# Performance work log

Hardware: AMD Instinct MI355X
Metric: run time of the kernel (lower is better)

The kernel has to match this reference:

```python
import jax, jax.numpy as jnp
import numpy as np

N, E, T = 4096, 49152, 262144
H, EMB, AIN, EB, TB = 256, 64, 92, 80, 40
NBLK = 12  # 4 alignn * 2 EGGC + 4 gcn


def _ln(x, s, b):
    mu = jnp.mean(x, -1, keepdims=True)
    v = jnp.mean((x - mu) ** 2, -1, keepdims=True)
    return (x - mu) * jax.lax.rsqrt(v + 1e-5) * s + b


def _mlp(x, W, b, s, bi):
    # Linear -> LayerNorm -> SiLU (MLPLayer)
    return jax.nn.silu(_ln(x @ W + b, s, bi))


def _rbf(x, vmin, vmax, bins):
    centers = jnp.linspace(vmin, vmax, bins)
    gamma = 1.0 / ((vmax - vmin) / (bins - 1))
    return jnp.exp(-gamma * (x[:, None] - centers) ** 2)


def _eggc(x, e, src, dst, W, b, ln_s, ln_b, n_nodes):
    # W: [5,H,H] = src_gate, dst_gate, edge_gate, src_update, dst_update
    m = (x @ W[0] + b[0])[src] + (x @ W[1] + b[1])[dst] + (e @ W[2] + b[2])
    sigma = jax.nn.sigmoid(m)
    sum_sh = jax.ops.segment_sum((x @ W[4] + b[4])[src] * sigma, dst, num_segments=n_nodes)
    sum_s = jax.ops.segment_sum(sigma, dst, num_segments=n_nodes)
    h = sum_sh / (sum_s + 1e-6)
    x_new = jax.nn.silu(_ln(x @ W[3] + b[3] + h, ln_s[0], ln_b[0]))
    e_new = jax.nn.silu(_ln(m, ln_s[1], ln_b[1]))
    return x + x_new, e + e_new  # residual=True


def setup_inputs() -> dict:
    key = jax.random.key(0)
    ks = jax.random.split(key, 16)
    s = 0.05
    return {
        "atom_features": jax.random.normal(ks[0], (N, AIN), jnp.float32),
        "r": jax.random.normal(ks[1], (E, 3), jnp.float32),
        "src": jax.random.randint(ks[2], (E,), 0, N),
        "dst": jax.random.randint(ks[3], (E,), 0, N),
        "lsrc": jax.random.randint(ks[4], (T,), 0, E),
        "ldst": jax.random.randint(ks[5], (T,), 0, E),
        "atom_W": s * jax.random.normal(ks[6], (AIN, H), jnp.float32),
        "atom_b": jnp.zeros((H,), jnp.float32),
        "atom_ln_s": jnp.ones((H,), jnp.float32),
        "atom_ln_b": jnp.zeros((H,), jnp.float32),
        "edge_W1": s * jax.random.normal(ks[7], (EB, EMB), jnp.float32),
        "edge_b1": jnp.zeros((EMB,), jnp.float32),
        "edge_ln1_s": jnp.ones((EMB,), jnp.float32),
        "edge_ln1_b": jnp.zeros((EMB,), jnp.float32),
        "edge_W2": s * jax.random.normal(ks[8], (EMB, H), jnp.float32),
        "edge_b2": jnp.zeros((H,), jnp.float32),
        "edge_ln2_s": jnp.ones((H,), jnp.float32),
        "edge_ln2_b": jnp.zeros((H,), jnp.float32),
        "ang_W1": s * jax.random.normal(ks[9], (TB, EMB), jnp.float32),
        "ang_b1": jnp.zeros((EMB,), jnp.float32),
        "ang_ln1_s": jnp.ones((EMB,), jnp.float32),
        "ang_ln1_b": jnp.zeros((EMB,), jnp.float32),
        "ang_W2": s * jax.random.normal(ks[10], (EMB, H), jnp.float32),
        "ang_b2": jnp.zeros((H,), jnp.float32),
        "ang_ln2_s": jnp.ones((H,), jnp.float32),
        "ang_ln2_b": jnp.zeros((H,), jnp.float32),
        "eggc_W": s * jax.random.normal(ks[11], (NBLK, 5, H, H), jnp.float32),
        "eggc_b": jnp.zeros((NBLK, 5, H), jnp.float32),
        "eggc_ln_s": jnp.ones((NBLK, 2, H), jnp.float32),
        "eggc_ln_b": jnp.zeros((NBLK, 2, H), jnp.float32),
        "fc_W": s * jax.random.normal(ks[12], (H, 1), jnp.float32),
        "fc_b": jnp.zeros((1,), jnp.float32),
    }


def reference(atom_features, r, src, dst, lsrc, ldst,
              atom_W, atom_b, atom_ln_s, atom_ln_b,
              edge_W1, edge_b1, edge_ln1_s, edge_ln1_b,
              edge_W2, edge_b2, edge_ln2_s, edge_ln2_b,
              ang_W1, ang_b1, ang_ln1_s, ang_ln1_b,
              ang_W2, ang_b2, ang_ln2_s, ang_ln2_b,
              eggc_W, eggc_b, eggc_ln_s, eggc_ln_b, fc_W, fc_b):
    # line-graph bond cosines: cos(-r_i, r_j) for each bond pair
    r1, r2 = -r[lsrc], r[ldst]
    cos = jnp.sum(r1 * r2, -1) / (jnp.linalg.norm(r1, axis=-1) * jnp.linalg.norm(r2, axis=-1))
    cos = jnp.clip(cos, -1.0, 1.0)
    z = _mlp(_mlp(_rbf(cos, -1.0, 1.0, TB), ang_W1, ang_b1, ang_ln1_s, ang_ln1_b),
             ang_W2, ang_b2, ang_ln2_s, ang_ln2_b)
    x = _mlp(atom_features, atom_W, atom_b, atom_ln_s, atom_ln_b)
    bondlength = jnp.linalg.norm(r, axis=1)
    y = _mlp(_mlp(_rbf(bondlength, 0.0, 8.0, EB), edge_W1, edge_b1, edge_ln1_s, edge_ln1_b),
             edge_W2, edge_b2, edge_ln2_s, edge_ln2_b)
    for i in range(4):  # alignn layers: crystal graph then line graph
        x, m = _eggc(x, y, src, dst, eggc_W[2 * i], eggc_b[2 * i], eggc_ln_s[2 * i], eggc_ln_b[2 * i], N)
        y, z = _eggc(m, z, lsrc, ldst, eggc_W[2 * i + 1], eggc_b[2 * i + 1], eggc_ln_s[2 * i + 1], eggc_ln_b[2 * i + 1], E)
    for i in range(4):  # gcn layers
        j = 8 + i
        x, y = _eggc(x, y, src, dst, eggc_W[j], eggc_b[j], eggc_ln_s[j], eggc_ln_b[j], N)
    atomwise_energy = x @ fc_W + fc_b  # [N,1]
    total_energy = jnp.mean(atomwise_energy)  # AvgPooling (eV/atom), single graph
    return total_energy, atomwise_energy
```

## Files before the change

kernel.cpp:

```cpp
#include <hip/hip_runtime.h>


typedef unsigned short bfu;
typedef __attribute__((ext_vector_type(8))) short short8;
typedef __attribute__((ext_vector_type(4))) float floatx4;

#define CHN 4096
#define CHCAP 24576
#define HH 65536

__device__ __forceinline__ float bf2f(bfu u) {
  union { unsigned u; float f; } x; x.u = ((unsigned)u) << 16; return x.f;
}
__device__ __forceinline__ bfu f2bf(float f) {
  union { float f; unsigned u; } x; x.f = f;
  unsigned r = x.u + 0x7FFFu + ((x.u >> 16) & 1u);
  return (bfu)(r >> 16);
}
__device__ __forceinline__ float fsig(float x) {
  return __builtin_amdgcn_rcpf(1.f + __expf(-x));
}
__device__ __forceinline__ float fsilu(float x) { return x * fsig(x); }

struct f8 { float v[8]; };
__device__ __forceinline__ f8 ld8(const bfu* p) {
  short8 u = *(const short8*)(const void*)p;
  f8 r;
#pragma unroll
  for (int i = 0; i < 8; ++i) r.v[i] = bf2f((bfu)u[i]);
  return r;
}
__device__ __forceinline__ void st8(bfu* p, f8 x) {
  short8 u;
#pragma unroll
  for (int i = 0; i < 8; ++i) u[i] = (short)f2bf(x.v[i]);
  *(short8*)(void*)p = u;
}
__device__ __forceinline__ f8 add8(f8 a, f8 b) {
  f8 r;
#pragma unroll
  for (int i = 0; i < 8; ++i) r.v[i] = a.v[i] + b.v[i];
  return r;
}
__device__ __forceinline__ f8 sig8(f8 m) {
  f8 r;
#pragma unroll
  for (int i = 0; i < 8; ++i) r.v[i] = fsig(m.v[i]);
  return r;
}
__device__ __forceinline__ void wstats32(const f8& x, float& mean, float& rstd) {
  float s = 0.f, q = 0.f;
#pragma unroll
  for (int i = 0; i < 8; ++i) { s += x.v[i]; q += x.v[i] * x.v[i]; }
#pragma unroll
  for (int m = 1; m < 32; m <<= 1) { s += __shfl_xor(s, m); q += __shfl_xor(q, m); }
  mean = s * (1.f / 256.f);
  rstd = rsqrtf(fmaxf(q * (1.f / 256.f) - mean * mean, 0.f) + 1e-5f);
}
__device__ __forceinline__ f8 lnsilu8(f8 pre, f8 sg, f8 bb) {
  float mean, rstd; wstats32(pre, mean, rstd);
  f8 r;
#pragma unroll
  for (int i = 0; i < 8; ++i)
    r.v[i] = fsilu((pre.v[i] - mean) * rstd * sg.v[i] + bb.v[i]);
  return r;
}

__device__ __forceinline__ float block_sum256(float t, float* sm) {
#pragma unroll
  for (int o = 32; o; o >>= 1) t += __shfl_down(t, o);
  if ((threadIdx.x & 63) == 0) sm[threadIdx.x >> 6] = t;
  __syncthreads();
  float r = sm[0] + sm[1] + sm[2] + sm[3];
  __syncthreads();
  return r;
}

__global__ void probe_kernel(const unsigned* __restrict__ ones_raw, int* __restrict__ mode) {
  if (threadIdx.x == 0) *mode = (ones_raw[0] == 0x3F800000u) ? 1 : 0;
}
__global__ __launch_bounds__(256) void cvt_kernel(
    const void* __restrict__ src, bfu* __restrict__ dst, int n, const int* __restrict__ mode) {
  int i = blockIdx.x * 256 + threadIdx.x;
  if (i >= n) return;
  dst[i] = (*mode) ? f2bf(((const float*)src)[i]) : ((const bfu*)src)[i];
}
__global__ __launch_bounds__(256) void cvtf_kernel(
    const void* __restrict__ src, float* __restrict__ dst, int n, const int* __restrict__ mode) {
  int i = blockIdx.x * 256 + threadIdx.x;
  if (i >= n) return;
  dst[i] = (*mode) ? ((const float*)src)[i] : bf2f(((const bfu*)src)[i]);
}
struct CvtDesc { const void* src; bfu* dst; int n; };
struct CvtPack { CvtDesc e[20]; };
__global__ __launch_bounds__(256) void cvt_batch_kernel(CvtPack p, const int* __restrict__ mode) {
  CvtDesc d = p.e[blockIdx.y];
  int i = blockIdx.x * 256 + threadIdx.x;
  if (i >= d.n) return;
  d.dst[i] = (*mode) ? f2bf(((const float*)d.src)[i]) : ((const bfu*)d.src)[i];
}

template<int BM, int BN, int WR, int WC>
__device__ __forceinline__ void gemm_body(
    const bfu* __restrict__ A, const bfu* __restrict__ Bt,
    const bfu* __restrict__ bias, bfu* __restrict__ Cout,
    int cnt, int N, int K, int base, int m0, int n0)
{
  constexpr int WM = BM / WR, WN = BN / WC;
  constexpr int TM = WM / 16, TN = WN / 16;
  constexpr int LDT = 72;
  static __shared__ bfu As[BM * LDT];
  static __shared__ bfu Bs[BN * LDT];

  const int tid = threadIdx.x, wave = tid >> 6, lane = tid & 63;
  const int wr = wave / WC, wc = wave % WC;
  const int lrow = lane & 15, kq = (lane >> 4) * 8;

  floatx4 acc[TM][TN];
#pragma unroll
  for (int i = 0; i < TM; ++i)
#pragma unroll
    for (int j = 0; j < TN; ++j) acc[i][j] = (floatx4){0.f, 0.f, 0.f, 0.f};

  constexpr int ACH = BM * 8, BCH = BN * 8;
  for (int k0 = 0; k0 < K; k0 += 64) {
#pragma unroll
    for (int idx = tid; idx < ACH; idx += 256) {
      int row = idx >> 3, kc = (idx & 7) << 3;
      int r = m0 + row;
      int ar = base + (r < cnt ? r : cnt - 1);
      *(short8*)(void*)(As + row * LDT + kc) =
          *(const short8*)(const void*)(A + (size_t)ar * K + k0 + kc);
    }
#pragma unroll
    for (int idx = tid; idx < BCH; idx += 256) {
      int row = idx >> 3, kc = (idx & 7) << 3;
      *(short8*)(void*)(Bs + row * LDT + kc) =
          *(const short8*)(const void*)(Bt + (size_t)(n0 + row) * K + k0 + kc);
    }
    __syncthreads();
#pragma unroll
    for (int s = 0; s < 2; ++s) {
      short8 Af[TM], Bf[TN];
#pragma unroll
      for (int i = 0; i < TM; ++i)
        Af[i] = *(const short8*)(const void*)(As + (wr * WM + i * 16 + lrow) * LDT + s * 32 + kq);
#pragma unroll
      for (int j = 0; j < TN; ++j)
        Bf[j] = *(const short8*)(const void*)(Bs + (wc * WN + j * 16 + lrow) * LDT + s * 32 + kq);
#pragma unroll
      for (int i = 0; i < TM; ++i)
#pragma unroll
        for (int j = 0; j < TN; ++j)
          acc[i][j] = __builtin_amdgcn_mfma_f32_16x16x32_bf16(Af[i], Bf[j], acc[i][j], 0, 0, 0);
    }
    __syncthreads();
  }

  const int rquad = lane >> 4, cin = lane & 15;
#pragma unroll
  for (int i = 0; i < TM; ++i) {
#pragma unroll
    for (int rr = 0; rr < 4; ++rr) {
      int orow = m0 + wr * WM + i * 16 + rquad * 4 + rr;
      if (orow >= cnt) continue;
#pragma unroll
      for (int j = 0; j < TN; ++j) {
        int gcol = n0 + wc * WN + j * 16 + cin;
        Cout[(size_t)orow * N + gcol] = f2bf(acc[i][j][rr] + bf2f(bias[gcol]));
      }
    }
  }
}

template<int BM, int BN, int WR, int WC>
__global__ __launch_bounds__(256) void gemm_kernel(
    const bfu* __restrict__ A, const bfu* __restrict__ Bt,
    const bfu* __restrict__ bias, bfu* __restrict__ Cout, int M, int N, int K)
{
  gemm_body<BM, BN, WR, WC>(A, Bt, bias, Cout, M, N, K, 0,
                            blockIdx.x * BM, blockIdx.y * BN);
}

__global__ __launch_bounds__(256) void line_gemm_kernel(
    const bfu* __restrict__ z, const bfu* __restrict__ yb,
    const bfu* __restrict__ W, const bfu* __restrict__ bb,
    bfu* __restrict__ mchunk, bfu* __restrict__ u3c,
    const int* __restrict__ loff, int n0, int n1)
{
  if (blockIdx.y < 2) {
    int base = loff[n0], cnt = loff[n1] - base;
    int m0 = blockIdx.x * 128;
    if (m0 >= cnt) return;
    gemm_body<128, 128, 2, 2>(z, W + 4 * HH, bb + 4 * 256, mchunk,
                              cnt, 256, 256, base, m0, blockIdx.y * 128);
  } else {
    if (blockIdx.x >= 64) return;
    gemm_body<128, 128, 2, 2>(yb + (size_t)n0 * 256, W + 3 * HH, bb + 3 * 256, u3c,
                              CHN, 256, 256, 0, (blockIdx.x & 31) * 128, (blockIdx.x >> 5) * 128);
  }
}

__global__ __launch_bounds__(256) void atom_gemm_kernel(
    const bfu* __restrict__ x, const bfu* __restrict__ y,
    const bfu* __restrict__ W, const bfu* __restrict__ bb,
    bfu* __restrict__ afused, bfu* __restrict__ mbufa)
{
  if (blockIdx.x < 384) {
    gemm_body<128, 128, 2, 2>(y, W + 4 * HH, bb + 4 * 256, mbufa,
                              49152, 256, 256, 0, blockIdx.x * 128, blockIdx.y * 128);
  } else {
    int lid = (blockIdx.x - 384) * 2 + blockIdx.y;
    gemm_body<128, 128, 2, 2>(x, W, bb, afused,
                              4096, 1024, 256, 0, (lid >> 3) * 128, (lid & 7) * 128);
  }
}

__global__ __launch_bounds__(256) void line_gates_kernel(
    const bfu* __restrict__ y, const bfu* __restrict__ z,
    const bfu* __restrict__ W, const bfu* __restrict__ bb,
    bfu* __restrict__ lfused, bfu* __restrict__ mchunk, bfu* __restrict__ u3c,
    const int* __restrict__ loff)
{
  if (blockIdx.y < 6) {
    gemm_body<128, 128, 2, 2>(y, W, bb, lfused,
                              49152, 768, 256, 0, blockIdx.x * 128, blockIdx.y * 128);
  } else if (blockIdx.y < 8) {
    int cnt = loff[CHN];
    int m0 = blockIdx.x * 128;
    if (blockIdx.x >= CHCAP / 128 || m0 >= cnt) return;
    gemm_body<128, 128, 2, 2>(z, W + 4 * HH, bb + 4 * 256, mchunk,
                              cnt, 256, 256, 0, m0, (blockIdx.y - 6) * 128);
  } else {
    if (blockIdx.x >= 64) return;
    gemm_body<128, 128, 2, 2>(y, W + 3 * HH, bb + 3 * 256, u3c,
                              CHN, 256, 256, 0, (blockIdx.x & 31) * 128, (blockIdx.x >> 5) * 128);
  }
}

__global__ __launch_bounds__(256) void cosbl_kernel(
    const float* __restrict__ r, const int* __restrict__ lsrc_p,
    const int* __restrict__ ldst_p, float* __restrict__ cosv,
    float* __restrict__ bl, int T, int E)
{
  int idx = blockIdx.x * 256 + threadIdx.x;
  if (idx < T) {
    int e1 = lsrc_p[idx], e2 = ldst_p[idx];
    float ax = -r[e1 * 3 + 0], ay = -r[e1 * 3 + 1], az = -r[e1 * 3 + 2];
    float bx =  r[e2 * 3 + 0], by =  r[e2 * 3 + 1], bz =  r[e2 * 3 + 2];
    float dot = ax * bx + ay * by + az * bz;
    float na = sqrtf(ax * ax + ay * ay + az * az);
    float nb = sqrtf(bx * bx + by * by + bz * bz);
    float c = dot / (na * nb);
    cosv[idx] = fminf(1.f, fmaxf(-1.f, c));
  } else if (idx < T + E) {
    int e = idx - T;
    float x = r[e * 3 + 0], yv = r[e * 3 + 1], zv = r[e * 3 + 2];
    bl[e] = sqrtf(x * x + yv * yv + zv * zv);
  }
}

template<int KP, int BINS, int IS_ANG>
__global__ __launch_bounds__(256) void mlp1_ln_kernel(
    const float* __restrict__ v, const bfu* __restrict__ Bt,
    const bfu* __restrict__ bias, const bfu* __restrict__ lns,
    const bfu* __restrict__ lnb, bfu* __restrict__ outp, int M)
{
  constexpr int LDT = KP + 8;
  __shared__ bfu As[128 * LDT];
  const int tid = threadIdx.x, wave = tid >> 6, lane = tid & 63;
  const int lrow = lane & 15, kq = (lane >> 4) * 8;
  const int m0 = blockIdx.x * 128;

  for (int idx = tid; idx < 128 * (KP / 8); idx += 256) {
    int row = idx / (KP / 8), kc = (idx % (KP / 8)) * 8;
    float val = v[m0 + row];
    short8 pack;
#pragma unroll
    for (int jj = 0; jj < 8; ++jj) {
      int k = kc + jj;
      float e = 0.f;
      if (k < BINS) {
        float center = IS_ANG ? (-1.f + k * (2.f / 39.f)) : (k * (8.f / 79.f));
        float d = val - center;
        e = __expf((IS_ANG ? -19.5f : -9.875f) * d * d);
      }
      pack[jj] = (short)f2bf(e);
    }
    *(short8*)(void*)(As + row * LDT + kc) = pack;
  }
  __syncthreads();

  floatx4 acc[2][4];
#pragma unroll
  for (int i = 0; i < 2; ++i)
#pragma unroll
    for (int j = 0; j < 4; ++j) acc[i][j] = (floatx4){0.f, 0.f, 0.f, 0.f};
#pragma unroll
  for (int ks = 0; ks < KP / 32; ++ks) {
    short8 Af[2], Bf[4];
#pragma unroll
    for (int j = 0; j < 4; ++j)
      Bf[j] = *(const short8*)(const void*)(Bt + (size_t)(j * 16 + lrow) * KP + ks * 32 + kq);
#pragma unroll
    for (int i = 0; i < 2; ++i)
      Af[i] = *(const short8*)(const void*)(As + (wave * 32 + i * 16 + lrow) * LDT + ks * 32 + kq);
#pragma unroll
    for (int i = 0; i < 2; ++i)
#pragma unroll
      for (int j = 0; j < 4; ++j)
        acc[i][j] = __builtin_amdgcn_mfma_f32_16x16x32_bf16(Af[i], Bf[j], acc[i][j], 0, 0, 0);
  }

  const int rquad = lane >> 4, cin = lane & 15;
  float bj[4], sj[4], lj[4];
#pragma unroll
  for (int j = 0; j < 4; ++j) {
    bj[j] = bf2f(bias[j * 16 + cin]);
    sj[j] = bf2f(lns[j * 16 + cin]);
    lj[j] = bf2f(lnb[j * 16 + cin]);
  }
#pragma unroll
  for (int i = 0; i < 2; ++i) {
#pragma unroll
    for (int rr = 0; rr < 4; ++rr) {
      int row = m0 + wave * 32 + i * 16 + rquad * 4 + rr;
      float pre[4], s = 0.f, q = 0.f;
#pragma unroll
      for (int j = 0; j < 4; ++j) {
        pre[j] = acc[i][j][rr] + bj[j];
        s += pre[j]; q += pre[j] * pre[j];
      }
#pragma unroll
      for (int mm = 1; mm < 16; mm <<= 1) { s += __shfl_xor(s, mm); q += __shfl_xor(q, mm); }
      float mean = s * (1.f / 64.f);
      float rstd = rsqrtf(fmaxf(q * (1.f / 64.f) - mean * mean, 0.f) + 1e-5f);
#pragma unroll
      for (int j = 0; j < 4; ++j) {
        float u = (pre[j] - mean) * rstd * sj[j] + lj[j];
        outp[(size_t)row * 64 + j * 16 + cin] = f2bf(fsilu(u));
      }
    }
  }
}

__global__ __launch_bounds__(256) void mlp2_ln_kernel(
    const bfu* __restrict__ A, const bfu* __restrict__ Bt,
    const bfu* __restrict__ bias, const bfu* __restrict__ lns,
    const bfu* __restrict__ lnb, bfu* __restrict__ outp, int M)
{
  __shared__ bfu As[64 * 72];
  __shared__ float part[64 * 8];
  const int tid = threadIdx.x, wave = tid >> 6, lane = tid & 63;
  const int lrow = lane & 15, kq = (lane >> 4) * 8;
  const int m0 = blockIdx.x * 64;

  short8 Bf[2][4];
#pragma unroll
  for (int s = 0; s < 2; ++s)
#pragma unroll
    for (int j = 0; j < 4; ++j)
      Bf[s][j] = *(const short8*)(const void*)(
          Bt + (size_t)(wave * 64 + j * 16 + lrow) * 64 + s * 32 + kq);

  for (int idx = tid; idx < 512; idx += 256) {
    int row = idx >> 3, kc = (idx & 7) << 3;
    *(short8*)(void*)(As + row * 72 + kc) =
        *(const short8*)(const void*)(A + (size_t)(m0 + row) * 64 + kc);
  }
  __syncthreads();

  floatx4 acc[4][4];
#pragma unroll
  for (int i = 0; i < 4; ++i)
#pragma unroll
    for (int j = 0; j < 4; ++j) acc[i][j] = (floatx4){0.f, 0.f, 0.f, 0.f};
#pragma unroll
  for (int s = 0; s < 2; ++s) {
    short8 Af[4];
#pragma unroll
    for (int i = 0; i < 4; ++i)
      Af[i] = *(const short8*)(const void*)(As + (i * 16 + lrow) * 72 + s * 32 + kq);
#pragma unroll
    for (int i = 0; i < 4; ++i)
#pragma unroll
      for (int j = 0; j < 4; ++j)
        acc[i][j] = __builtin_amdgcn_mfma_f32_16x16x32_bf16(Af[i], Bf[s][j], acc[i][j], 0, 0, 0);
  }

  const int rquad = lane >> 4, cin = lane & 15;
  float bj[4], sj[4], lj[4];
#pragma unroll
  for (int j = 0; j < 4; ++j) {
    int col = wave * 64 + j * 16 + cin;
    bj[j] = bf2f(bias[col]); sj[j] = bf2f(lns[col]); lj[j] = bf2f(lnb[col]);
  }
#pragma unroll
  for (int i = 0; i < 4; ++i) {
#pragma unroll
    for (int rr = 0; rr < 4; ++rr) {
      float s = 0.f, q = 0.f;
#pragma unroll
      for (int j = 0; j < 4; ++j) {
        float p = acc[i][j][rr] + bj[j];
        s += p; q += p * p;
      }
#pragma unroll
      for (int mm = 1; mm < 16; mm <<= 1) { s += __shfl_xor(s, mm); q += __shfl_xor(q, mm); }
      if (cin == 0) {
        int row = i * 16 + rquad * 4 + rr;
        part[row * 8 + wave * 2] = s;
        part[row * 8 + wave * 2 + 1] = q;
      }
    }
  }
  __syncthreads();
#pragma unroll
  for (int i = 0; i < 4; ++i) {
#pragma unroll
    for (int rr = 0; rr < 4; ++rr) {
      int row = i * 16 + rquad * 4 + rr;
      float s = part[row * 8] + part[row * 8 + 2] + part[row * 8 + 4] + part[row * 8 + 6];
      float q = part[row * 8 + 1] + part[row * 8 + 3] + part[row * 8 + 5] + part[row * 8 + 7];
      float mean = s * (1.f / 256.f);
      float rstd = rsqrtf(fmaxf(q * (1.f / 256.f) - mean * mean, 0.f) + 1e-5f);
#pragma unroll
      for (int j = 0; j < 4; ++j) {
        float u = (acc[i][j][rr] + bj[j] - mean) * rstd * sj[j] + lj[j];
        outp[(size_t)(m0 + row) * 256 + wave * 64 + j * 16 + cin] = f2bf(fsilu(u));
      }
    }
  }
}

__global__ __launch_bounds__(256) void count_kernel(
    const int* __restrict__ d, int* __restrict__ cnt, int ne) {
  int i = blockIdx.x * 256 + threadIdx.x;
  if (i < ne) atomicAdd(&cnt[d[i]], 1);
}
__global__ __launch_bounds__(256) void scan_kernel(
    const int* __restrict__ cnt, int* __restrict__ off, int n) {
  __shared__ int ssum[256];
  __shared__ int sbase[257];
  int t = threadIdx.x;
  int strip = (n + 255) / 256;
  int lo = t * strip, hi = lo + strip; if (hi > n) hi = n; if (lo > n) lo = n;
  int s = 0;
  for (int i = lo; i < hi; ++i) s += cnt[i];
  ssum[t] = s;
  __syncthreads();
  if (t == 0) {
    int run = 0;
    for (int i = 0; i < 256; ++i) { sbase[i] = run; run += ssum[i]; }
    sbase[256] = run;
  }
  __syncthreads();
  int run = sbase[t];
  for (int i = lo; i < hi; ++i) { off[i] = run; run += cnt[i]; }
  if (t == 0) off[n] = sbase[256];
}
__global__ __launch_bounds__(256) void copy_kernel(
    const int* __restrict__ a, int* __restrict__ b, int n) {
  int i = blockIdx.x * 256 + threadIdx.x;
  if (i < n) b[i] = a[i];
}
__global__ __launch_bounds__(256) void fill_kernel(
    const int* __restrict__ d, int* __restrict__ cur, int* __restrict__ ids, int ne) {
  int i = blockIdx.x * 256 + threadIdx.x;
  if (i < ne) ids[atomicAdd(&cur[d[i]], 1)] = i;
}
__global__ __launch_bounds__(256) void fill2_kernel(
    const int* __restrict__ ldst, const int* __restrict__ lsrc, int* __restrict__ cur,
    int* __restrict__ lsrc_p, int* __restrict__ ldst_p, int ne) {
  int i = blockIdx.x * 256 + threadIdx.x;
  if (i >= ne) return;
  int d = ldst[i];
  int pos = atomicAdd(&cur[d], 1);
  lsrc_p[pos] = lsrc[i];
  ldst_p[pos] = d;
}

__global__ __launch_bounds__(256) void transpose_pad_kernel(
    const void* __restrict__ W, bfu* __restrict__ Wt, int K, int N, int Kp,
    const int* __restrict__ mode)
{
  int idx = blockIdx.x * 256 + threadIdx.x;
  if (idx >= N * Kp) return;
  int n = idx / Kp, k = idx - n * Kp;
  bfu v = 0;
  if (k < K) {
    size_t si = (size_t)k * N + n;
    v = (*mode) ? f2bf(((const float*)W)[si]) : ((const bfu*)W)[si];
  }
  Wt[idx] = v;
}
__device__ __forceinline__ int slot2mat(int slot) {
  const int m[5] = {0, 4, 1, 3, 2};
  return m[slot];
}
__global__ __launch_bounds__(256) void transpose_eggc_kernel(
    const void* __restrict__ W, bfu* __restrict__ Wt, const int* __restrict__ mode)
{
  int bs = blockIdx.y;
  int blk = bs / 5, slot = bs - blk * 5;
  int mat = slot2mat(slot);
  int idx = blockIdx.x * 256 + threadIdx.x;
  int n = idx >> 8, k = idx & 255;
  size_t si = ((size_t)(blk * 5 + mat) * 256 + k) * 256 + n;
  bfu v = (*mode) ? f2bf(((const float*)W)[si]) : ((const bfu*)W)[si];
  Wt[((size_t)bs * 256 + n) * 256 + k] = v;
}
__global__ __launch_bounds__(256) void bias_perm_kernel(
    const void* __restrict__ B, bfu* __restrict__ Bp, const int* __restrict__ mode)
{
  int i = blockIdx.x * 256 + threadIdx.x;
  int bs = i >> 8, c = i & 255;
  int blk = bs / 5, slot = bs - blk * 5;
  int mat = slot2mat(slot);
  size_t si = (size_t)(blk * 5 + mat) * 256 + c;
  Bp[i] = (*mode) ? f2bf(((const float*)B)[si]) : ((const bfu*)B)[si];
}

__global__ __launch_bounds__(256) void atom_fused_kernel(
    const bfu* __restrict__ mbuf, const bfu* __restrict__ af,
    const int* __restrict__ src, const int* __restrict__ dst,
    bfu* __restrict__ X, bfu* __restrict__ Y,
    const int* __restrict__ aoff, const int* __restrict__ aids,
    int eblk,
    const bfu* __restrict__ lns, const bfu* __restrict__ lnb,
    const bfu* __restrict__ les, const bfu* __restrict__ leb)
{
  int wave = threadIdx.x >> 6, lane = threadIdx.x & 63;
  int half = lane >> 5, c8 = (lane & 31) * 8;
  if ((int)blockIdx.x < eblk) {
    int e = blockIdx.x * 8 + wave * 2 + half;
    f8 m = add8(add8(ld8(mbuf + (size_t)e * 256 + c8),
                     ld8(af + (size_t)src[e] * 1024 + c8)),
                ld8(af + (size_t)dst[e] * 1024 + 512 + c8));
    f8 sil = lnsilu8(m, ld8(les + c8), ld8(leb + c8));
    bfu* op = Y + (size_t)e * 256 + c8;
    st8(op, add8(sil, ld8(op)));
  } else {
    int n = (blockIdx.x - eblk) * 4 + wave;
    int p0 = aoff[n], p1 = aoff[n + 1];
    f8 g1 = ld8(af + (size_t)n * 1024 + 512 + c8);
    f8 num = {}, den = {};
    for (int p = p0 + half; p < p1; p += 2) {
      int id = aids[p], sx = src[id];
      f8 m = add8(add8(ld8(mbuf + (size_t)id * 256 + c8),
                       ld8(af + (size_t)sx * 1024 + c8)), g1);
      f8 sg = sig8(m);
      f8 u4 = ld8(af + (size_t)sx * 1024 + 256 + c8);
#pragma unroll
      for (int i = 0; i < 8; ++i) {
        num.v[i] += sg.v[i] * u4.v[i];
        den.v[i] += sg.v[i];
      }
    }
#pragma unroll
    for (int i = 0; i < 8; ++i) {
      num.v[i] += __shfl_xor(num.v[i], 32);
      den.v[i] += __shfl_xor(den.v[i], 32);
    }
    f8 u3 = ld8(af + (size_t)n * 1024 + 768 + c8);
    f8 pre;
#pragma unroll
    for (int i = 0; i < 8; ++i)
      pre.v[i] = u3.v[i] + num.v[i] / (den.v[i] + 1e-6f);
    f8 sil = lnsilu8(pre, ld8(lns + c8), ld8(lnb + c8));
    if (half == 0) {
      bfu* op = X + (size_t)n * 256 + c8;
      st8(op, add8(sil, ld8(op)));
    }
  }
}

__global__ __launch_bounds__(256) void line_fused_kernel(
    const bfu* __restrict__ mchunk, const bfu* __restrict__ lf,
    const bfu* __restrict__ u3c,
    const int* __restrict__ loff, const int* __restrict__ lsrc_p,
    const int* __restrict__ ldst_p,
    bfu* __restrict__ Z, bfu* __restrict__ Y,
    int n0, int eblk,
    const bfu* __restrict__ lns, const bfu* __restrict__ lnb,
    const bfu* __restrict__ les, const bfu* __restrict__ leb)
{
  int wave = threadIdx.x >> 6, lane = threadIdx.x & 63;
  int half = lane >> 5, c8 = (lane & 31) * 8;
  int base = loff[n0];
  if ((int)blockIdx.x < eblk) {
    int rloc = blockIdx.x * 8 + wave * 2 + half;
    int cnt = loff[n0 + CHN] - base;
    if (rloc >= cnt) return;
    int p = base + rloc;
    f8 m = add8(add8(ld8(mchunk + (size_t)rloc * 256 + c8),
                     ld8(lf + (size_t)lsrc_p[p] * 768 + c8)),
                ld8(lf + (size_t)ldst_p[p] * 768 + 512 + c8));
    f8 sil = lnsilu8(m, ld8(les + c8), ld8(leb + c8));
    bfu* op = Z + (size_t)p * 256 + c8;
    st8(op, add8(sil, ld8(op)));
  } else {
    int n = n0 + (blockIdx.x - eblk) * 4 + wave;
    int p0 = loff[n], p1 = loff[n + 1];
    f8 g1 = ld8(lf + (size_t)n * 768 + 512 + c8);
    f8 num = {}, den = {};
    for (int p = p0 + half; p < p1; p += 2) {
      int sx = lsrc_p[p];
      f8 m = add8(add8(ld8(mchunk + (size_t)(p - base) * 256 + c8),
                       ld8(lf + (size_t)sx * 768 + c8)), g1);
      f8 sg = sig8(m);
      f8 u4 = ld8(lf + (size_t)sx * 768 + 256 + c8);
#pragma unroll
      for (int i = 0; i < 8; ++i) {
        num.v[i] += sg.v[i] * u4.v[i];
        den.v[i] += sg.v[i];
      }
    }
#pragma unroll
    for (int i = 0; i < 8; ++i) {
      num.v[i] += __shfl_xor(num.v[i], 32);
      den.v[i] += __shfl_xor(den.v[i], 32);
    }
    f8 u3 = ld8(u3c + (size_t)(n - n0) * 256 + c8);
    f8 pre;
#pragma unroll
    for (int i = 0; i < 8; ++i)
      pre.v[i] = u3.v[i] + num.v[i] / (den.v[i] + 1e-6f);
    f8 sil = lnsilu8(pre, ld8(lns + c8), ld8(lnb + c8));
    if (half == 0) {
      bfu* op = Y + (size_t)n * 256 + c8;
      st8(op, add8(sil, ld8(op)));
    }
  }
}

__global__ __launch_bounds__(256) void atom_init_kernel(
    const bfu* __restrict__ af, const bfu* __restrict__ W, const bfu* __restrict__ bias,
    const bfu* __restrict__ lns, const bfu* __restrict__ lnb, bfu* __restrict__ X)
{
  __shared__ float sm[4];
  int row = blockIdx.x, c = threadIdx.x;
  float acc = bf2f(bias[c]);
  for (int k = 0; k < 92; ++k)
    acc += bf2f(af[row * 92 + k]) * bf2f(W[k * 256 + c]);
  float mean = block_sum256(acc, sm) * (1.f / 256.f);
  float d = acc - mean;
  float var = block_sum256(d * d, sm) * (1.f / 256.f);
  float u = d * rsqrtf(var + 1e-5f) * bf2f(lns[c]) + bf2f(lnb[c]);
  X[(size_t)row * 256 + c] = f2bf(fsilu(u));
}

__global__ __launch_bounds__(256) void final_kernel(
    const bfu* __restrict__ X, const bfu* __restrict__ fcW, const bfu* __restrict__ fcb,
    void* __restrict__ out, float* __restrict__ acc, const int* __restrict__ mode)
{
  int row = blockIdx.x * 4 + (threadIdx.x >> 6);
  int lane = threadIdx.x & 63;
  float s = 0.f;
#pragma unroll
  for (int k = 0; k < 4; ++k)
    s += bf2f(X[(size_t)row * 256 + lane + k * 64]) * bf2f(fcW[lane + k * 64]);
#pragma unroll
  for (int o = 32; o; o >>= 1) s += __shfl_down(s, o);
  if (lane == 0) {
    float v = s + bf2f(fcb[0]);
    if (*mode) ((float*)out)[1 + row] = v;
    else       ((bfu*)out)[1 + row] = f2bf(v);
    atomicAdd(acc, v);
  }
}
__global__ void mean_kernel(const float* __restrict__ acc, void* __restrict__ out,
                            const int* __restrict__ mode) {
  if (threadIdx.x == 0) {
    float v = acc[0] * (1.f / 4096.f);
    if (*mode) ((float*)out)[0] = v;
    else       ((bfu*)out)[0] = f2bf(v);
  }
}
__global__ void dbg_kernel(void* __restrict__ out, float v) {
  if (threadIdx.x == 0) { ((bfu*)out)[0] = f2bf(v); }
}

static void gemm128(const bfu* A, const bfu* Bt, const bfu* bias, bfu* C,
                    int M, int N, int K, hipStream_t st) {
  dim3 g(M / 128, N / 128);
  gemm_kernel<128, 128, 2, 2><<<g, 256, 0, st>>>(A, Bt, bias, C, M, N, K);
}

extern "C" void kernel_launch(void* const* d_in, const int* in_sizes, int n_in,
                              void* d_out, int out_size, void* d_ws, size_t ws_size,
                              hipStream_t stream) {
  const int N = 4096, E = 49152, T = 262144, H = 256;

  const int* src  = (const int*)d_in[2];
  const int* dst  = (const int*)d_in[3];
  const int* lsrc = (const int*)d_in[4];
  const int* ldst = (const int*)d_in[5];

  char* bp = (char*)d_ws;
  size_t off = 0;
  auto carve = [&](size_t bytes) -> char* {
    char* q = bp + off;
    off = (off + bytes + 255) & ~(size_t)255;
    return q;
  };
  bfu* x       = (bfu*)carve((size_t)N * H * 2);
  bfu* y       = (bfu*)carve((size_t)E * H * 2);
  bfu* z       = (bfu*)carve((size_t)T * H * 2);
  bfu* reg     = (bfu*)carve((size_t)E * 768 * 2);
  bfu* u3c     = (bfu*)carve((size_t)CHN * H * 2);
  bfu* mchunk  = (bfu*)carve((size_t)CHCAP * H * 2);
  bfu* WtE     = (bfu*)carve((size_t)60 * H * H * 2);
  bfu* ebp     = (bfu*)carve((size_t)12 * 5 * H * 2);
  bfu* Wt_a1   = (bfu*)carve(64 * 64 * 2);
  bfu* Wt_a2   = (bfu*)carve(256 * 64 * 2);
  bfu* Wt_e1   = (bfu*)carve(64 * 128 * 2);
  bfu* Wt_e2   = (bfu*)carve(256 * 64 * 2);
  int* aoff    = (int*)carve((size_t)(N + 1) * 4);
  int* aids    = (int*)carve((size_t)E * 4);
  int* loff    = (int*)carve((size_t)(E + 1) * 4);
  int* lsrc_p  = (int*)carve((size_t)T * 4);
  int* ldst_p  = (int*)carve((size_t)T * 4);
  int* cursors = (int*)carve((size_t)E * 4);
  float* macc  = (float*)carve(256);
  int* mode    = (int*)carve(256);
  bfu* par_c   = (bfu*)carve(8192 * 2);
  bfu* els_c   = (bfu*)carve((size_t)12 * 2 * H * 2);
  bfu* elb_c   = (bfu*)carve((size_t)12 * 2 * H * 2);

  if (off > ws_size) {
    hipMemsetAsync(d_out, 0, (size_t)out_size * 2, stream);
    dbg_kernel<<<1, 64, 0, stream>>>(d_out, (float)(ws_size >> 20));
    return;
  }

  char* tail = (char*)reg + (size_t)52 * 1024 * 1024;
  bfu* af_c  = (bfu*)tail;                 tail += ((size_t)N * 92 * 2 + 255) & ~255ull;
  float* r_f = (float*)tail;               tail += ((size_t)E * 3 * 4 + 255) & ~255ull;
  float* cosv = (float*)tail;              tail += ((size_t)T * 4 + 255) & ~255ull;
  float* blv = (float*)tail;               tail += ((size_t)E * 4 + 255) & ~255ull;
  bfu* atW_c = (bfu*)tail;

  bfu* atom_b_c   = par_c + 0;
  bfu* atom_lns_c = par_c + 256;
  bfu* atom_lnb_c = par_c + 512;
  bfu* e_b1_c     = par_c + 768;
  bfu* e_l1s_c    = par_c + 832;
  bfu* e_l1b_c    = par_c + 896;
  bfu* e_b2_c     = par_c + 1024;
  bfu* e_l2s_c    = par_c + 1280;
  bfu* e_l2b_c    = par_c + 1536;
  bfu* a_b1_c     = par_c + 1792;
  bfu* a_l1s_c    = par_c + 1856;
  bfu* a_l1b_c    = par_c + 1920;
  bfu* a_b2_c     = par_c + 2048;
  bfu* a_l2s_c    = par_c + 2304;
  bfu* a_l2b_c    = par_c + 2560;
  bfu* fcW_c      = par_c + 2816;
  bfu* fcb_c      = par_c + 3072;

  bfu* lfused = reg;
  bfu* afused = reg;
  bfu* mbufa  = reg + (size_t)N * 1024;
  bfu* emb_t  = reg;
  bfu* emb_e  = reg + (size_t)T * 64;

  probe_kernel<<<1, 64, 0, stream>>>((const unsigned*)d_in[8], mode);
  CvtPack pk;
  int ii = 0;
  auto add = [&](int idx, bfu* dstp, int n) { pk.e[ii++] = {d_in[idx], dstp, n}; };
  add(7, atom_b_c, 256);  add(8, atom_lns_c, 256); add(9, atom_lnb_c, 256);
  add(11, e_b1_c, 64);    add(12, e_l1s_c, 64);    add(13, e_l1b_c, 64);
  add(15, e_b2_c, 256);   add(16, e_l2s_c, 256);   add(17, e_l2b_c, 256);
  add(19, a_b1_c, 64);    add(20, a_l1s_c, 64);    add(21, a_l1b_c, 64);
  add(23, a_b2_c, 256);   add(24, a_l2s_c, 256);   add(25, a_l2b_c, 256);
  add(30, fcW_c, 256);    add(31, fcb_c, 1);
  add(28, els_c, 12 * 2 * 256);
  add(29, elb_c, 12 * 2 * 256);
  add(6, atW_c, 92 * 256);
  cvt_batch_kernel<<<dim3(92, 20), 256, 0, stream>>>(pk, mode);
  cvt_kernel<<<(N * 92 + 255) / 256, 256, 0, stream>>>(d_in[0], af_c, N * 92, mode);
  cvtf_kernel<<<(E * 3 + 255) / 256, 256, 0, stream>>>(d_in[1], r_f, E * 3, mode);

  hipMemsetAsync(cursors, 0, (size_t)N * 4, stream);
  count_kernel<<<E / 256, 256, 0, stream>>>(dst, cursors, E);
  scan_kernel<<<1, 256, 0, stream>>>(cursors, aoff, N);
  copy_kernel<<<(N + 255) / 256, 256, 0, stream>>>(aoff, cursors, N);
  fill_kernel<<<E / 256, 256, 0, stream>>>(dst, cursors, aids, E);

  hipMemsetAsync(cursors, 0, (size_t)E * 4, stream);
  count_kernel<<<T / 256, 256, 0, stream>>>(ldst, cursors, T);
  scan_kernel<<<1, 256, 0, stream>>>(cursors, loff, E);
  copy_kernel<<<(E + 255) / 256, 256, 0, stream>>>(loff, cursors, E);
  fill2_kernel<<<T / 256, 256, 0, stream>>>(ldst, lsrc, cursors, lsrc_p, ldst_p, T);

  transpose_eggc_kernel<<<dim3(256, 60), 256, 0, stream>>>(d_in[26], WtE, mode);
  bias_perm_kernel<<<60, 256, 0, stream>>>(d_in[27], ebp, mode);
  transpose_pad_kernel<<<16, 256, 0, stream>>>(d_in[18], Wt_a1, 40, 64, 64, mode);
  transpose_pad_kernel<<<64, 256, 0, stream>>>(d_in[22], Wt_a2, 64, 256, 64, mode);
  transpose_pad_kernel<<<32, 256, 0, stream>>>(d_in[10], Wt_e1, 80, 64, 128, mode);
  transpose_pad_kernel<<<64, 256, 0, stream>>>(d_in[14], Wt_e2, 64, 256, 64, mode);

  cosbl_kernel<<<(T + E + 255) / 256, 256, 0, stream>>>(r_f, lsrc_p, ldst_p, cosv, blv, T, E);
  mlp1_ln_kernel<64, 40, 1><<<T / 128, 256, 0, stream>>>(
      cosv, Wt_a1, a_b1_c, a_l1s_c, a_l1b_c, emb_t, T);
  mlp2_ln_kernel<<<T / 64, 256, 0, stream>>>(emb_t, Wt_a2, a_b2_c, a_l2s_c, a_l2b_c, z, T);
  mlp1_ln_kernel<128, 80, 0><<<E / 128, 256, 0, stream>>>(
      blv, Wt_e1, e_b1_c, e_l1s_c, e_l1b_c, emb_e, E);
  mlp2_ln_kernel<<<E / 64, 256, 0, stream>>>(emb_e, Wt_e2, e_b2_c, e_l2s_c, e_l2b_c, y, E);

  atom_init_kernel<<<N, 256, 0, stream>>>(af_c, atW_c, atom_b_c, atom_lns_c, atom_lnb_c, x);

  auto atom_eggc = [&](int blk, int do_edge) {
    const bfu* W  = WtE + (size_t)blk * 5 * HH;
    const bfu* bb = ebp + (size_t)blk * 5 * H;
    const bfu* ls = els_c + (size_t)blk * 2 * H;
    const bfu* lb = elb_c + (size_t)blk * 2 * H;
    atom_gemm_kernel<<<dim3(512, 2), 256, 0, stream>>>(x, y, W, bb, afused, mbufa);
    int eblk = do_edge ? E / 8 : 0;
    atom_fused_kernel<<<eblk + N / 4, 256, 0, stream>>>(
        mbufa, afused, src, dst, x, y, aoff, aids, eblk, ls, lb, ls + H, lb + H);
  };

  auto line_eggc = [&](int blk, int do_edge) {
    const bfu* W  = WtE + (size_t)blk * 5 * HH;
    const bfu* bb = ebp + (size_t)blk * 5 * H;
    const bfu* ls = els_c + (size_t)blk * 2 * H;
    const bfu* lb = elb_c + (size_t)blk * 2 * H;
    line_gates_kernel<<<dim3(384, 9), 256, 0, stream>>>(
        y, z, W, bb, lfused, mchunk, u3c, loff);
    for (int c = 0; c < E / CHN; ++c) {
      int n0 = c * CHN;
      int eblk = do_edge ? CHCAP / 8 : 0;
      line_fused_kernel<<<eblk + CHN / 4, 256, 0, stream>>>(
          mchunk, lfused, u3c, loff, lsrc_p, ldst_p, z, y, n0, eblk,
          ls, lb, ls + H, lb + H);
      if (c + 1 < E / CHN)
        line_gemm_kernel<<<dim3(CHCAP / 128, 3), 256, 0, stream>>>(
            z, y, W, bb, mchunk, u3c, loff, n0 + CHN, n0 + 2 * CHN);
    }
  };

  for (int i = 0; i < 4; ++i) {
    atom_eggc(2 * i, 1);
    line_eggc(2 * i + 1, i < 3);
  }
  for (int i = 0; i < 4; ++i)
    atom_eggc(8 + i, i < 3);

  hipMemsetAsync(macc, 0, 4, stream);
  final_kernel<<<N / 4, 256, 0, stream>>>(x, fcW_c, fcb_c, d_out, macc, mode);
  mean_kernel<<<1, 64, 0, stream>>>(macc, d_out, mode);
}
```

Baseline: 2.870 ms.

## Fuse line-graph chunk elementwise pass with next chunk's GEMM, double-buffered

Replaces the alternating line_fused and line_gemm launches with a single line_step kernel. Its blocks do the gather, sigmoid, aggregation and LayerNorm work for chunk c while other blocks compute the edge-gate and update GEMMs for chunk c+1 into the other half of double-buffered mchunk and u3c buffers. Chunk size is halved (CHN 4096→2048, CHCAP scaled to match), giving 24 steps. The intent is to overlap the memory-bound elementwise work with the GEMM and remove the serialization between the two kernels, at the cost of more steps and the same per-chunk capacity assumption.

```diff
diff --git a/kernel.cpp b/kernel.cpp
--- a/kernel.cpp
+++ b/kernel.cpp
@@ -5,8 +5,8 @@
 typedef __attribute__((ext_vector_type(8))) short short8;
 typedef __attribute__((ext_vector_type(4))) float floatx4;
 
-#define CHN 4096
-#define CHCAP 24576
+#define CHN 2048
+#define CHCAP 12288
 #define HH 65536
 
 __device__ __forceinline__ float bf2f(bfu u) {
@@ -182,25 +182,6 @@
                             blockIdx.x * BM, blockIdx.y * BN);
 }
 
-__global__ __launch_bounds__(256) void line_gemm_kernel(
-    const bfu* __restrict__ z, const bfu* __restrict__ yb,
-    const bfu* __restrict__ W, const bfu* __restrict__ bb,
-    bfu* __restrict__ mchunk, bfu* __restrict__ u3c,
-    const int* __restrict__ loff, int n0, int n1)
-{
-  if (blockIdx.y < 2) {
-    int base = loff[n0], cnt = loff[n1] - base;
-    int m0 = blockIdx.x * 128;
-    if (m0 >= cnt) return;
-    gemm_body<128, 128, 2, 2>(z, W + 4 * HH, bb + 4 * 256, mchunk,
-                              cnt, 256, 256, base, m0, blockIdx.y * 128);
-  } else {
-    if (blockIdx.x >= 64) return;
-    gemm_body<128, 128, 2, 2>(yb + (size_t)n0 * 256, W + 3 * HH, bb + 3 * 256, u3c,
-                              CHN, 256, 256, 0, (blockIdx.x & 31) * 128, (blockIdx.x >> 5) * 128);
-  }
-}
-
 __global__ __launch_bounds__(256) void atom_gemm_kernel(
     const bfu* __restrict__ x, const bfu* __restrict__ y,
     const bfu* __restrict__ W, const bfu* __restrict__ bb,
@@ -219,7 +200,7 @@
 __global__ __launch_bounds__(256) void line_gates_kernel(
     const bfu* __restrict__ y, const bfu* __restrict__ z,
     const bfu* __restrict__ W, const bfu* __restrict__ bb,
-    bfu* __restrict__ lfused, bfu* __restrict__ mchunk, bfu* __restrict__ u3c,
+    bfu* __restrict__ lfused, bfu* __restrict__ mch0, bfu* __restrict__ u3c0,
     const int* __restrict__ loff)
 {
   if (blockIdx.y < 6) {
@@ -229,12 +210,92 @@
     int cnt = loff[CHN];
     int m0 = blockIdx.x * 128;
     if (blockIdx.x >= CHCAP / 128 || m0 >= cnt) return;
-    gemm_body<128, 128, 2, 2>(z, W + 4 * HH, bb + 4 * 256, mchunk,
+    gemm_body<128, 128, 2, 2>(z, W + 4 * HH, bb + 4 * 256, mch0,
                               cnt, 256, 256, 0, m0, (blockIdx.y - 6) * 128);
   } else {
-    if (blockIdx.x >= 64) return;
-    gemm_body<128, 128, 2, 2>(y, W + 3 * HH, bb + 3 * 256, u3c,
-                              CHN, 256, 256, 0, (blockIdx.x & 31) * 128, (blockIdx.x >> 5) * 128);
+    if (blockIdx.x >= 32) return;
+    gemm_body<128, 128, 2, 2>(y, W + 3 * HH, bb + 3 * 256, u3c0,
+                              CHN, 256, 256, 0, (blockIdx.x & 15) * 128, (blockIdx.x >> 4) * 128);
+  }
+}
+
+__global__ __launch_bounds__(256) void line_step_kernel(
+    const bfu* __restrict__ z, const bfu* __restrict__ yb,
+    const bfu* __restrict__ lf, const bfu* __restrict__ W, const bfu* __restrict__ bb,
+    const bfu* __restrict__ mA, bfu* __restrict__ mB,
+    const bfu* __restrict__ u3A, bfu* __restrict__ u3B,
+    const int* __restrict__ loff, const int* __restrict__ lsrc_p,
+    const int* __restrict__ ldst_p,
+    bfu* __restrict__ Z, bfu* __restrict__ Y,
+    int n0, int eblk, int do_gemm,
+    const bfu* __restrict__ lns, const bfu* __restrict__ lnb,
+    const bfu* __restrict__ les, const bfu* __restrict__ leb)
+{
+  const int nblk = CHN / 4;
+  int bx = blockIdx.x;
+  if (bx < eblk + nblk) {
+    int wave = threadIdx.x >> 6, lane = threadIdx.x & 63;
+    int half = lane >> 5, c8 = (lane & 31) * 8;
+    int base = loff[n0];
+    if (bx < eblk) {
+      int rloc = bx * 8 + wave * 2 + half;
+      int cnt = loff[n0 + CHN] - base;
+      if (rloc >= cnt) return;
+      int p = base + rloc;
+      f8 m = add8(add8(ld8(mA + (size_t)rloc * 256 + c8),
+                       ld8(lf + (size_t)lsrc_p[p] * 768 + c8)),
+                  ld8(lf + (size_t)ldst_p[p] * 768 + 512 + c8));
+      f8 sil = lnsilu8(m, ld8(les + c8), ld8(leb + c8));
+      bfu* op = Z + (size_t)p * 256 + c8;
+      st8(op, add8(sil, ld8(op)));
+    } else {
+      int n = n0 + (bx - eblk) * 4 + wave;
+      int p0 = loff[n], p1 = loff[n + 1];
+      f8 g1 = ld8(lf + (size_t)n * 768 + 512 + c8);
+      f8 num = {}, den = {};
+      for (int p = p0 + half; p < p1; p += 2) {
+        int sx = lsrc_p[p];
+        f8 m = add8(add8(ld8(mA + (size_t)(p - base) * 256 + c8),
+                         ld8(lf + (size_t)sx * 768 + c8)), g1);
+        f8 sg = sig8(m);
+        f8 u4 = ld8(lf + (size_t)sx * 768 + 256 + c8);
+#pragma unroll
+        for (int i = 0; i < 8; ++i) {
+          num.v[i] += sg.v[i] * u4.v[i];
+          den.v[i] += sg.v[i];
+        }
+      }
+#pragma unroll
+      for (int i = 0; i < 8; ++i) {
+        num.v[i] += __shfl_xor(num.v[i], 32);
+        den.v[i] += __shfl_xor(den.v[i], 32);
+      }
+      f8 u3 = ld8(u3A + (size_t)(n - n0) * 256 + c8);
+      f8 pre;
+#pragma unroll
+      for (int i = 0; i < 8; ++i)
+        pre.v[i] = u3.v[i] + num.v[i] / (den.v[i] + 1e-6f);
+      f8 sil = lnsilu8(pre, ld8(lns + c8), ld8(lnb + c8));
+      if (half == 0) {
+        bfu* op = Y + (size_t)n * 256 + c8;
+        st8(op, add8(sil, ld8(op)));
+      }
+    }
+  } else {
+    if (!do_gemm) return;
+    int gb = bx - (eblk + nblk);
+    int n1 = n0 + CHN;
+    if (gb < (CHCAP / 128) * 2) {
+      int base = loff[n1], cnt = loff[n1 + CHN] - base;
+      int m0 = (gb >> 1) * 128;
+      if (m0 >= cnt) return;
+      gemm_body<128, 128, 2, 2>(z, W + 4 * HH, bb + 4 * 256, mB,
+                                cnt, 256, 256, base, m0, (gb & 1) * 128);
+    } else {
+      int ub = gb - (CHCAP / 128) * 2;
+      gemm_body<128, 128, 2, 2>(yb + (size_t)n1 * 256, W + 3 * HH, bb + 3 * 256, u3B,
+                                CHN, 256, 256, 0, (ub & 15) * 128, (ub >> 4) * 128);
+    }
   }
 }
 
@@ -575,65 +636,6 @@
   }
 }
 
-__global__ __launch_bounds__(256) void line_fused_kernel(
-    const bfu* __restrict__ mchunk, const bfu* __restrict__ lf,
-    const bfu* __restrict__ u3c,
-    const int* __restrict__ loff, const int* __restrict__ lsrc_p,
-    const int* __restrict__ ldst_p,
-    bfu* __restrict__ Z, bfu* __restrict__ Y,
-    int n0, int eblk,
-    const bfu* __restrict__ lns, const bfu* __restrict__ lnb,
-    const bfu* __restrict__ les, const bfu* __restrict__ leb)
-{
-  int wave = threadIdx.x >> 6, lane = threadIdx.x & 63;
-  int half = lane >> 5, c8 = (lane & 31) * 8;
-  int base = loff[n0];
-  if ((int)blockIdx.x < eblk) {
-    int rloc = blockIdx.x * 8 + wave * 2 + half;
-    int cnt = loff[n0 + CHN] - base;
-    if (rloc >= cnt) return;
-    int p = base + rloc;
-    f8 m = add8(add8(ld8(mchunk + (size_t)rloc * 256 + c8),
-                     ld8(lf + (size_t)lsrc_p[p] * 768 + c8)),
-                ld8(lf + (size_t)ldst_p[p] * 768 + 512 + c8));
-    f8 sil = lnsilu8(m, ld8(les + c8), ld8(leb + c8));
-    bfu* op = Z + (size_t)p * 256 + c8;
-    st8(op, add8(sil, ld8(op)));
-  } else {
-    int n = n0 + (blockIdx.x - eblk) * 4 + wave;
-    int p0 = loff[n], p1 = loff[n + 1];
-    f8 g1 = ld8(lf + (size_t)n * 768 + 512 + c8);
-    f8 num = {}, den = {};
-    for (int p = p0 + half; p < p1; p += 2) {
-      int sx = lsrc_p[p];
-      f8 m = add8(add8(ld8(mchunk + (size_t)(p - base) * 256 + c8),
-                       ld8(lf + (size_t)sx * 768 + c8)), g1);
-      f8 sg = sig8(m);
-      f8 u4 = ld8(lf + (size_t)sx * 768 + 256 + c8);
-#pragma unroll
-      for (int i = 0; i < 8; ++i) {
-        num.v[i] += sg.v[i] * u4.v[i];
-        den.v[i] += sg.v[i];
-      }
-    }
-#pragma unroll
-    for (int i = 0; i < 8; ++i) {
-      num.v[i] += __shfl_xor(num.v[i], 32);
-      den.v[i] += __shfl_xor(den.v[i], 32);
-    }
-    f8 u3 = ld8(u3c + (size_t)(n - n0) * 256 + c8);
-    f8 pre;
-#pragma unroll
-    for (int i = 0; i < 8; ++i)
-      pre.v[i] = u3.v[i] + num.v[i] / (den.v[i] + 1e-6f);
-    f8 sil = lnsilu8(pre, ld8(lns + c8), ld8(lnb + c8));
-    if (half == 0) {
-      bfu* op = Y + (size_t)n * 256 + c8;
-      st8(op, add8(sil, ld8(op)));
-    }
-  }
-}
-
 __global__ __launch_bounds__(256) void atom_init_kernel(
     const bfu* __restrict__ af, const bfu* __restrict__ W, const bfu* __restrict__ bias,
     const bfu* __restrict__ lns, const bfu* __restrict__ lnb, bfu* __restrict__ X)
@@ -708,8 +710,8 @@
   bfu* y       = (bfu*)carve((size_t)E * H * 2);
   bfu* z       = (bfu*)carve((size_t)T * H * 2);
   bfu* reg     = (bfu*)carve((size_t)E * 768 * 2);
-  bfu* u3c     = (bfu*)carve((size_t)CHN * H * 2);
-  bfu* mchunk  = (bfu*)carve((size_t)CHCAP * H * 2);
+  bfu* u3c     = (bfu*)carve((size_t)2 * CHN * H * 2);
+  bfu* mchunk  = (bfu*)carve((size_t)2 * CHCAP * H * 2);
   bfu* WtE     = (bfu*)carve((size_t)60 * H * H * 2);
   bfu* ebp     = (bfu*)carve((size_t)12 * 5 * H * 2);
   bfu* Wt_a1   = (bfu*)carve(64 * 64 * 2);
@@ -829,15 +831,18 @@
     const bfu* lb = elb_c + (size_t)blk * 2 * H;
     line_gates_kernel<<<dim3(384, 9), 256, 0, stream>>>(
         y, z, W, bb, lfused, mchunk, u3c, loff);
-    for (int c = 0; c < E / CHN; ++c) {
+    for (int c = 0; c < 24; ++c) {
       int n0 = c * CHN;
+      const bfu* mA = mchunk + (size_t)(c & 1) * CHCAP * 256;
+      bfu* mB = mchunk + (size_t)((c + 1) & 1) * CHCAP * 256;
+      const bfu* u3A = u3c + (size_t)(c & 1) * CHN * 256;
+      bfu* u3B = u3c + (size_t)((c + 1) & 1) * CHN * 256;
       int eblk = do_edge ? CHCAP / 8 : 0;
-      line_fused_kernel<<<eblk + CHN / 4, 256, 0, stream>>>(
-          mchunk, lfused, u3c, loff, lsrc_p, ldst_p, z, y, n0, eblk,
-          ls, lb, ls + H, lb + H);
-      if (c + 1 < E / CHN)
-        line_gemm_kernel<<<dim3(CHCAP / 128, 3), 256, 0, stream>>>(
-            z, y, W, bb, mchunk, u3c, loff, n0 + CHN, n0 + 2 * CHN);
+      int do_gemm = (c < 23);
+      int grid = eblk + CHN / 4 + (CHCAP / 128) * 2 + 32;
+      line_step_kernel<<<grid, 256, 0, stream>>>(
+          z, y, lfused, W, bb, mA, mB, u3A, u3B, loff, lsrc_p, ldst_p,
+          z, y, n0, eblk, do_gemm, ls, lb, ls + H, lb + H);
     }
   };
 
```

Result: slower. 3.616 ms (+26.0%).
